# Optimization experiments

Measured on AMD Instinct MI355X. Metric: run time of the kernel, lower is better.

The kernel has to match this reference:

```python
import jax, jax.numpy as jnp
import numpy as np

B, S, D, H = 2, 2048, 1024, 16
DK = D // H

def setup_inputs() -> dict:
    key = jax.random.key(0)
    ks = jax.random.split(key, 12)
    s = 1.0 / np.sqrt(D)
    return {
        "q": jax.random.normal(ks[0], (B, S, D), jnp.float32),
        "k": jax.random.normal(ks[1], (B, S, D), jnp.float32),
        "v": jax.random.normal(ks[2], (B, S, D), jnp.float32),
        "mask": jnp.ones((1, 1, S, S), jnp.int32),
        "Wq": jax.random.normal(ks[3], (D, D), jnp.float32) * s,
        "bq": jnp.zeros((D,), jnp.float32),
        "Wk": jax.random.normal(ks[4], (D, D), jnp.float32) * s,
        "bk": jnp.zeros((D,), jnp.float32),
        "Wv": jax.random.normal(ks[5], (D, D), jnp.float32) * s,
        "bv": jnp.zeros((D,), jnp.float32),
        "Wo": jax.random.normal(ks[6], (D, D), jnp.float32) * s,
        "bo": jnp.zeros((D,), jnp.float32),
    }

def reference(q, k, v, mask, Wq, bq, Wk, bk, Wv, bv, Wo, bo):
    # projections (torch Linear: x @ W^T + b)
    Q = q @ Wq.T + bq
    K = k @ Wk.T + bk
    V = v @ Wv.T + bv
    # split heads: [B,S,D] -> [B,H,S,DK]
    def split(x):
        return x.reshape(B, S, H, DK).transpose(0, 2, 1, 3)
    Qh, Kh, Vh = split(Q), split(K), split(V)
    scores = jnp.einsum('bhqd,bhkd->bhqk', Qh, Kh) / jnp.sqrt(jnp.float32(DK))
    scores = jnp.where(mask == 0, jnp.float32(-1e9), scores)
    attn = jax.nn.softmax(scores, axis=-1)  # dropout p=0.0 -> identity
    x = jnp.einsum('bhqk,bhkd->bhqd', attn, Vh)
    x = x.transpose(0, 2, 1, 3).reshape(B, S, D)
    return x @ Wo.T + bo
```

## Files before the change

### kernel.cpp

```cpp
#include <hip/hip_runtime.h>
#include <hip/hip_bf16.h>
#include <stdint.h>

#define B_    2
#define S_    2048
#define D_    1024
#define H_    16
#define NTOK  (B_ * S_)

typedef __attribute__((ext_vector_type(8))) short bf16x8;
typedef __attribute__((ext_vector_type(4))) float f32x4;
typedef __attribute__((ext_vector_type(2))) float float2v;
typedef __attribute__((ext_vector_type(2))) __bf16 bfv2;

static __device__ __forceinline__ unsigned short f2bf(float f) {
    unsigned int u = __float_as_uint(f);
    unsigned int r = (u + 0x7FFFu + ((u >> 16) & 1u)) >> 16;
    return (unsigned short)r;
}
static __device__ __forceinline__ unsigned int pkbf(float a, float b) {
    float2v fv = {a, b};
    bfv2 r = __builtin_convertvector(fv, bfv2);
    unsigned int u;
    __builtin_memcpy(&u, &r, 4);
    return u;
}

using g_cu32 = __attribute__((address_space(1))) const unsigned int;
using l_u32  = __attribute__((address_space(3))) unsigned int;
static __device__ __forceinline__ void gld16(const void* g, void* l) {
    __builtin_amdgcn_global_load_lds((g_cu32*)g, (l_u32*)l, 16, 0, 0);
}

#define QN ((size_t)NTOK * D_)
#define WN ((size_t)D_ * D_)

__global__ __launch_bounds__(256) void prep_kernel(
    const float* __restrict__ q, const float* __restrict__ k, const float* __restrict__ v,
    const float* __restrict__ Wq, const float* __restrict__ Wk,
    const float* __restrict__ Wv, const float* __restrict__ Wo,
    const int* __restrict__ mask,
    unsigned short* __restrict__ qb, unsigned short* __restrict__ kb,
    unsigned short* __restrict__ vb, unsigned short* __restrict__ wqb,
    unsigned short* __restrict__ wkb, unsigned short* __restrict__ wvb,
    unsigned short* __restrict__ wob, int* __restrict__ flags) {
    __shared__ int anyz;
    if (blockIdx.x < 8192) {
        size_t i = ((size_t)blockIdx.x * 256 + threadIdx.x) * 8;
        const float* s; unsigned short* d; size_t off;
        if (i < QN)          { s = q; d = qb; off = i; }
        else if (i < 2 * QN) { s = k; d = kb; off = i - QN; }
        else if (i < 3 * QN) { s = v; d = vb; off = i - 2 * QN; }
        else {
            size_t j = i - 3 * QN;
            int wi = (int)(j >> 20);
            s = (wi == 0) ? Wq : (wi == 1) ? Wk : (wi == 2) ? Wv : Wo;
            d = (wi == 0) ? wqb : (wi == 1) ? wkb : (wi == 2) ? wvb : wob;
            off = j & (WN - 1);
        }
        float4 a = *(const float4*)(s + off);
        float4 b = *(const float4*)(s + off + 4);
        uint4 pk;
        pk.x = pkbf(a.x, a.y); pk.y = pkbf(a.z, a.w);
        pk.z = pkbf(b.x, b.y); pk.w = pkbf(b.z, b.w);
        *(uint4*)(d + off) = pk;
    } else {
        if (threadIdx.x == 0) anyz = 0;
        __syncthreads();
        int bid2 = blockIdx.x - 8192;
        const int qt = bid2 >> 5, kt = bid2 & 31;
        int az = 0;
        for (int i = threadIdx.x; i < 64 * 64; i += 256) {
            int r = i >> 6, c = i & 63;
            az |= (mask[(size_t)(qt * 64 + r) * S_ + kt * 64 + c] == 0) ? 1 : 0;
        }
        if (az) atomicOr(&anyz, 1);
        __syncthreads();
        if (threadIdx.x == 0) flags[qt * 32 + kt] = anyz;
    }
}

struct GemmArgs {
    const unsigned short* A[3];
    const unsigned short* W[3];
    const float* bias[3];
    void* C[3];
    int mode[3];
    float scale[3];
};

template<int BMT>
__global__ __launch_bounds__(256, 3) void gemm_async(GemmArgs ga) {
    constexpr int AG = BMT / 16;
    constexpr int MI = BMT / 32;
    const int z = blockIdx.z;
    const unsigned short* __restrict__ A = ga.A[z];
    const unsigned short* __restrict__ W = ga.W[z];
    const float* __restrict__ bias = ga.bias[z];
    void* C = ga.C[z];
    const int mode = ga.mode[z];
    const float scl = ga.scale[z];

    __shared__ unsigned short As[AG * 512];
    __shared__ unsigned short Bs[8 * 512];

    const int t    = threadIdx.x;
    const int lane = t & 63;
    const int w    = t >> 6;
    const int fr   = lane & 15;
    const int kq   = lane >> 4;
    const int wrow = w >> 1, wcol = w & 1;
    const int m0 = blockIdx.x * BMT, n0 = blockIdx.y * 128;

    const int sc = lane >> 4;
    const int sr = lane & 15;

    const unsigned short* ga0;
    const unsigned short* ga1 = nullptr;
    unsigned short* la0;
    unsigned short* la1 = nullptr;
    if constexpr (BMT == 128) {
        ga0 = A + (size_t)(m0 + (2 * w) * 16 + sr) * D_ + sc * 8;
        ga1 = ga0 + 16 * D_;
        la0 = &As[(2 * w) * 512];
        la1 = &As[(2 * w + 1) * 512];
    } else {
        ga0 = A + (size_t)(m0 + w * 16 + sr) * D_ + sc * 8;
        la0 = &As[w * 512];
    }
    const unsigned short* gw0 = W + (size_t)(n0 + (2 * w) * 16 + sr) * D_ + sc * 8;
    const unsigned short* gw1 = gw0 + 16 * D_;
    unsigned short* lw0 = &Bs[(2 * w) * 512];
    unsigned short* lw1 = &Bs[(2 * w + 1) * 512];

    int aOff[MI], bOff[4];
#pragma unroll
    for (int mi = 0; mi < MI; ++mi) aOff[mi] = (wrow * MI + mi) * 512 + (kq * 16 + fr) * 8;
#pragma unroll
    for (int ni = 0; ni < 4; ++ni) bOff[ni] = (wcol * 4 + ni) * 512 + (kq * 16 + fr) * 8;

    f32x4 acc[MI][4];
#pragma unroll
    for (int i = 0; i < MI; ++i)
#pragma unroll
        for (int j = 0; j < 4; ++j) acc[i][j] = (f32x4)0.0f;

    for (int k0 = 0; k0 < D_ / 32; ++k0) {
        gld16(ga0, la0);
        if constexpr (BMT == 128) gld16(ga1, la1);
        gld16(gw0, lw0);
        gld16(gw1, lw1);
        ga0 += 32; gw0 += 32; gw1 += 32;
        if constexpr (BMT == 128) ga1 += 32;
        __syncthreads();

        bf16x8 af[MI], bfr[4];
#pragma unroll
        for (int mi = 0; mi < MI; ++mi) af[mi] = *(const bf16x8*)&As[aOff[mi]];
#pragma unroll
        for (int ni = 0; ni < 4; ++ni) bfr[ni] = *(const bf16x8*)&Bs[bOff[ni]];
#pragma unroll
        for (int mi = 0; mi < MI; ++mi)
#pragma unroll
            for (int ni = 0; ni < 4; ++ni)
                acc[mi][ni] = __builtin_amdgcn_mfma_f32_16x16x32_bf16(
                    af[mi], bfr[ni], acc[mi][ni], 0, 0, 0);
        __syncthreads();
    }

    if (mode == 0) {
        float* Co = (float*)C;
#pragma unroll
        for (int ni = 0; ni < 4; ++ni) {
            int col = n0 + wcol * 64 + ni * 16 + fr;
            float bv = bias[col];
#pragma unroll
            for (int mi = 0; mi < MI; ++mi)
#pragma unroll
                for (int r = 0; r < 4; ++r) {
                    int row = m0 + wrow * (BMT / 2) + mi * 16 + kq * 4 + r;
                    Co[(size_t)row * D_ + col] = (acc[mi][ni][r] + bv) * scl;
                }
        }
    } else if (mode == 1) {
        unsigned short* Co = (unsigned short*)C;
#pragma unroll
        for (int ni = 0; ni < 4; ++ni) {
            int col = n0 + wcol * 64 + ni * 16 + fr;
            float bv = bias[col];
#pragma unroll
            for (int mi = 0; mi < MI; ++mi)
#pragma unroll
                for (int r = 0; r < 4; ++r) {
                    int row = m0 + wrow * (BMT / 2) + mi * 16 + kq * 4 + r;
                    Co[(size_t)row * D_ + col] = f2bf((acc[mi][ni][r] + bv) * scl);
                }
        }
    } else {
        unsigned short* Co = (unsigned short*)C;
#pragma unroll
        for (int ni = 0; ni < 4; ++ni) {
            int col = n0 + wcol * 64 + ni * 16 + fr;
            float bv = bias[col];
            int hh = col >> 6, d = col & 63;
#pragma unroll
            for (int mi = 0; mi < MI; ++mi) {
                int tok = m0 + wrow * (BMT / 2) + mi * 16 + kq * 4;
                int bb = tok >> 11, sbase = tok & (S_ - 1);
                uint2 pk;
                pk.x = pkbf((acc[mi][ni][0] + bv) * scl, (acc[mi][ni][1] + bv) * scl);
                pk.y = pkbf((acc[mi][ni][2] + bv) * scl, (acc[mi][ni][3] + bv) * scl);
                *(uint2*)(Co + ((size_t)((bb * H_ + hh) * 64 + d)) * S_ + sbase) = pk;
            }
        }
    }
}

__global__ __launch_bounds__(256, 4) void flash4(
    const unsigned short* __restrict__ Qb, const unsigned short* __restrict__ Kb,
    const unsigned short* __restrict__ Vtg, const int* __restrict__ mask,
    const int* __restrict__ flags, unsigned short* __restrict__ Xb) {
    __shared__ unsigned short Ks[2][4096];
    __shared__ unsigned short Vs[2][4096];
    __shared__ unsigned short Ps[4096];

    const int t    = threadIdx.x;
    const int lane = t & 63;
    const int w    = t >> 6;
    const int fr   = lane & 15;
    const int kq   = lane >> 4;
    const int qt = blockIdx.x, hd = blockIdx.y, b = blockIdx.z;
    const int q0 = qt * 64;
    const int swz = fr & 7;

    const unsigned short* qrow_p = Qb + (size_t)(b * S_ + q0 + w * 16 + fr) * D_ + hd * 64;
    bf16x8 qf[2];
    qf[0] = *(const bf16x8*)(qrow_p + kq * 8);
    qf[1] = *(const bf16x8*)(qrow_p + 32 + kq * 8);

    int fl = (lane < 32) ? flags[qt * 32 + lane] : 0;
    unsigned int fmask = (unsigned int)__ballot(fl != 0);

    const unsigned short* kbase =
        Kb + (size_t)(b * S_ + w * 16 + fr) * D_ + hd * 64 + kq * 8;
    const unsigned short* vbase =
        Vtg + ((size_t)((b * H_ + hd) * 64 + w * 16 + fr)) * S_ + kq * 8;

#pragma unroll
    for (int j = 0; j < 2; ++j) {
        gld16(kbase + j * 32, (char*)&Ks[0][0] + w * 2048 + j * 1024);
        gld16(vbase + j * 32, (char*)&Vs[0][0] + w * 2048 + j * 1024);
    }

    f32x4 o[4];
#pragma unroll
    for (int i = 0; i < 4; ++i) o[i] = (f32x4)0.0f;
    float l_i = 0.0f;

    for (int kt = 0; kt < 32; ++kt) {
        const int cur = kt & 1;
        __syncthreads();
        if (kt < 31) {
#pragma unroll
            for (int j = 0; j < 2; ++j) {
                gld16(kbase + (size_t)(kt + 1) * 64 * D_ + j * 32,
                      (char*)&Ks[cur ^ 1][0] + w * 2048 + j * 1024);
                gld16(vbase + (size_t)(kt + 1) * 64 + j * 32,
                      (char*)&Vs[cur ^ 1][0] + w * 2048 + j * 1024);
            }
        }

        f32x4 st[4];
#pragma unroll
        for (int mi = 0; mi < 4; ++mi) st[mi] = (f32x4)0.0f;
#pragma unroll
        for (int kk = 0; kk < 2; ++kk)
#pragma unroll
            for (int mi = 0; mi < 4; ++mi) {
                bf16x8 a = *(const bf16x8*)&Ks[cur][mi * 1024 + ((kk * 4 + kq) * 16 + fr) * 8];
                st[mi] = __builtin_amdgcn_mfma_f32_16x16x32_bf16(a, qf[kk], st[mi], 0, 0, 0);
            }

        if ((fmask >> kt) & 1u) {
#pragma unroll
            for (int mi = 0; mi < 4; ++mi) {
                int4 mv = *(const int4*)&mask[(size_t)(q0 + w * 16 + fr) * S_ + kt * 64 + mi * 16 + kq * 4];
                if (mv.x == 0) st[mi][0] = -3e8f;
                if (mv.y == 0) st[mi][1] = -3e8f;
                if (mv.z == 0) st[mi][2] = -3e8f;
                if (mv.w == 0) st[mi][3] = -3e8f;
            }
        }

#pragma unroll
        for (int mi = 0; mi < 4; ++mi) {
            float e0 = exp2f(st[mi][0]), e1 = exp2f(st[mi][1]);
            float e2 = exp2f(st[mi][2]), e3 = exp2f(st[mi][3]);
            l_i += (e0 + e1) + (e2 + e3);
            uint2 pk;
            pk.x = pkbf(e0, e1);
            pk.y = pkbf(e2, e3);
            int chunk = mi * 2 + (kq >> 1);
            *(uint2*)&Ps[(w * 16 + fr) * 64 + ((chunk ^ swz) << 3) + ((kq & 1) << 2)] = pk;
        }

#pragma unroll
        for (int kk = 0; kk < 2; ++kk) {
            int c = kk * 4 + kq;
            bf16x8 pb = *(const bf16x8*)&Ps[(w * 16 + fr) * 64 + ((c ^ swz) << 3)];
#pragma unroll
            for (int mi = 0; mi < 4; ++mi) {
                bf16x8 a = *(const bf16x8*)&Vs[cur][mi * 1024 + ((kk * 4 + kq) * 16 + fr) * 8];
                o[mi] = __builtin_amdgcn_mfma_f32_16x16x32_bf16(a, pb, o[mi], 0, 0, 0);
            }
        }
    }

    l_i += __shfl_xor(l_i, 16, 64);
    l_i += __shfl_xor(l_i, 32, 64);
    float rl = 1.0f / l_i;

#pragma unroll
    for (int mi = 0; mi < 4; ++mi) {
        uint2 pk;
        pk.x = pkbf(o[mi][0] * rl, o[mi][1] * rl);
        pk.y = pkbf(o[mi][2] * rl, o[mi][3] * rl);
        *(uint2*)(Xb + (size_t)(b * S_ + q0 + w * 16 + fr) * D_ + hd * 64 + mi * 16 + kq * 4) = pk;
    }
}

extern "C" void kernel_launch(void* const* d_in, const int* in_sizes, int n_in,
                              void* d_out, int out_size, void* d_ws, size_t ws_size,
                              hipStream_t stream) {
    const float* q    = (const float*)d_in[0];
    const float* k    = (const float*)d_in[1];
    const float* v    = (const float*)d_in[2];
    const int*   mask = (const int*)d_in[3];
    const float* Wq   = (const float*)d_in[4];
    const float* bq   = (const float*)d_in[5];
    const float* Wk   = (const float*)d_in[6];
    const float* bk   = (const float*)d_in[7];
    const float* Wv   = (const float*)d_in[8];
    const float* bv   = (const float*)d_in[9];
    const float* Wo   = (const float*)d_in[10];
    const float* bo   = (const float*)d_in[11];
    float* out = (float*)d_out;

    unsigned short* qb  = (unsigned short*)d_ws;
    unsigned short* kb  = qb + QN;
    unsigned short* vb  = kb + QN;
    unsigned short* Qf  = vb + QN;
    unsigned short* Kf  = Qf + QN;
    unsigned short* Vt  = Kf + QN;
    unsigned short* wqb = Vt + QN;
    unsigned short* wkb = wqb + WN;
    unsigned short* wvb = wkb + WN;
    unsigned short* wob = wvb + WN;
    int* flags = (int*)(wob + WN);

    const float SC = 0.18033688011112042f;

    prep_kernel<<<9216, 256, 0, stream>>>(q, k, v, Wq, Wk, Wv, Wo, mask,
                                          qb, kb, vb, wqb, wkb, wvb, wob, flags);

    GemmArgs g1;
    g1.A[0] = qb;  g1.W[0] = wqb; g1.bias[0] = bq; g1.C[0] = Qf; g1.mode[0] = 1; g1.scale[0] = SC;
    g1.A[1] = kb;  g1.W[1] = wkb; g1.bias[1] = bk; g1.C[1] = Kf; g1.mode[1] = 1; g1.scale[1] = 1.0f;
    g1.A[2] = vb;  g1.W[2] = wvb; g1.bias[2] = bv; g1.C[2] = Vt; g1.mode[2] = 2; g1.scale[2] = 1.0f;
    gemm_async<128><<<dim3(NTOK / 128, D_ / 128, 3), 256, 0, stream>>>(g1);

    flash4<<<dim3(S_ / 64, H_, B_), 256, 0, stream>>>(Qf, Kf, Vt, mask, flags, Qf);

    GemmArgs g2;
    g2.A[0] = Qf; g2.W[0] = wob; g2.bias[0] = bo; g2.C[0] = out; g2.mode[0] = 0; g2.scale[0] = 1.0f;
    g2.A[1] = g2.A[2] = nullptr; g2.W[1] = g2.W[2] = nullptr;
    g2.bias[1] = g2.bias[2] = nullptr; g2.C[1] = g2.C[2] = nullptr;
    g2.mode[1] = g2.mode[2] = 0; g2.scale[1] = g2.scale[2] = 1.0f;
    gemm_async<64><<<dim3(NTOK / 64, D_ / 128, 1), 256, 0, stream>>>(g2);
}
```

Baseline: 276.2 us.

## Enlarge attention blocks to 128 queries, swap GEMM MFMA operands for vector stores

The flash kernel now runs 512 threads (8 waves) per block covering 128 queries, so each staged K/V tile serves twice as many queries. Each wave loads one 16-byte chunk per tile, and the block index is remapped with a swizzle. Smaller edits switch to the hardware exp2, precompute the LDS P addresses and split the row-sum into a two-lane accumulator. In the GEMM, swapping the MFMA operands for modes 0 and 1 lets each lane write contiguous float4 or packed bf16 outputs and load bias as float4. The trade-offs are higher LDS use per block and a possible loss of occupancy.

```diff
diff --git a/kernel.cpp b/kernel.cpp
--- a/kernel.cpp
+++ b/kernel.cpp
@@ -13,11 +13,6 @@
 typedef __attribute__((ext_vector_type(2))) float float2v;
 typedef __attribute__((ext_vector_type(2))) __bf16 bfv2;
 
-static __device__ __forceinline__ unsigned short f2bf(float f) {
-    unsigned int u = __float_as_uint(f);
-    unsigned int r = (u + 0x7FFFu + ((u >> 16) & 1u)) >> 16;
-    return (unsigned short)r;
-}
 static __device__ __forceinline__ unsigned int pkbf(float a, float b) {
     float2v fv = {a, b};
     bfv2 r = __builtin_convertvector(fv, bfv2);
@@ -34,6 +29,9 @@
 
 #define QN ((size_t)NTOK * D_)
 #define WN ((size_t)D_ * D_)
+
+struct SwapT { static constexpr bool value = true; };
+struct NoSwapT { static constexpr bool value = false; };
 
 __global__ __launch_bounds__(256) void prep_kernel(
     const float* __restrict__ q, const float* __restrict__ k, const float* __restrict__ v,
@@ -145,58 +143,39 @@
 #pragma unroll
         for (int j = 0; j < 4; ++j) acc[i][j] = (f32x4)0.0f;
 
-    for (int k0 = 0; k0 < D_ / 32; ++k0) {
-        gld16(ga0, la0);
-        if constexpr (BMT == 128) gld16(ga1, la1);
-        gld16(gw0, lw0);
-        gld16(gw1, lw1);
-        ga0 += 32; gw0 += 32; gw1 += 32;
-        if constexpr (BMT == 128) ga1 += 32;
-        __syncthreads();
-
-        bf16x8 af[MI], bfr[4];
-#pragma unroll
-        for (int mi = 0; mi < MI; ++mi) af[mi] = *(const bf16x8*)&As[aOff[mi]];
-#pragma unroll
-        for (int ni = 0; ni < 4; ++ni) bfr[ni] = *(const bf16x8*)&Bs[bOff[ni]];
-#pragma unroll
-        for (int mi = 0; mi < MI; ++mi)
-#pragma unroll
-            for (int ni = 0; ni < 4; ++ni)
-                acc[mi][ni] = __builtin_amdgcn_mfma_f32_16x16x32_bf16(
-                    af[mi], bfr[ni], acc[mi][ni], 0, 0, 0);
-        __syncthreads();
-    }
-
-    if (mode == 0) {
-        float* Co = (float*)C;
-#pragma unroll
-        for (int ni = 0; ni < 4; ++ni) {
-            int col = n0 + wcol * 64 + ni * 16 + fr;
-            float bv = bias[col];
+    auto kloop = [&](auto swc) {
+        constexpr bool SW = decltype(swc)::value;
+        for (int k0 = 0; k0 < D_ / 32; ++k0) {
+            gld16(ga0, la0);
+            if constexpr (BMT == 128) gld16(ga1, la1);
+            gld16(gw0, lw0);
+            gld16(gw1, lw1);
+            ga0 += 32; gw0 += 32; gw1 += 32;
+            if constexpr (BMT == 128) ga1 += 32;
+            __syncthreads();
+
+            bf16x8 af[MI], bfr[4];
+#pragma unroll
+            for (int mi = 0; mi < MI; ++mi) af[mi] = *(const bf16x8*)&As[aOff[mi]];
+#pragma unroll
+            for (int ni = 0; ni < 4; ++ni) bfr[ni] = *(const bf16x8*)&Bs[bOff[ni]];
 #pragma unroll
             for (int mi = 0; mi < MI; ++mi)
 #pragma unroll
-                for (int r = 0; r < 4; ++r) {
-                    int row = m0 + wrow * (BMT / 2) + mi * 16 + kq * 4 + r;
-                    Co[(size_t)row * D_ + col] = (acc[mi][ni][r] + bv) * scl;
+                for (int ni = 0; ni < 4; ++ni) {
+                    if constexpr (SW)
+                        acc[mi][ni] = __builtin_amdgcn_mfma_f32_16x16x32_bf16(
+                            bfr[ni], af[mi], acc[mi][ni], 0, 0, 0);
+                    else
+                        acc[mi][ni] = __builtin_amdgcn_mfma_f32_16x16x32_bf16(
+                            af[mi], bfr[ni], acc[mi][ni], 0, 0, 0);
                 }
-        }
-    } else if (mode == 1) {
-        unsigned short* Co = (unsigned short*)C;
-#pragma unroll
-        for (int ni = 0; ni < 4; ++ni) {
-            int col = n0 + wcol * 64 + ni * 16 + fr;
-            float bv = bias[col];
-#pragma unroll
-            for (int mi = 0; mi < MI; ++mi)
-#pragma unroll
-                for (int r = 0; r < 4; ++r) {
-                    int row = m0 + wrow * (BMT / 2) + mi * 16 + kq * 4 + r;
-                    Co[(size_t)row * D_ + col] = f2bf((acc[mi][ni][r] + bv) * scl);
-                }
-        }
-    } else {
+            __syncthreads();
+        }
+    };
+    if (mode == 2) kloop(NoSwapT{}); else kloop(SwapT{});
+
+    if (mode == 2) {
         unsigned short* Co = (unsigned short*)C;
 #pragma unroll
         for (int ni = 0; ni < 4; ++ni) {
@@ -213,24 +192,58 @@
                 *(uint2*)(Co + ((size_t)((bb * H_ + hh) * 64 + d)) * S_ + sbase) = pk;
             }
         }
-    }
-}
-
-__global__ __launch_bounds__(256, 4) void flash4(
+    } else if (mode == 0) {
+        float* Co = (float*)C;
+#pragma unroll
+        for (int ni = 0; ni < 4; ++ni) {
+            int nb = n0 + wcol * 64 + ni * 16 + kq * 4;
+            float4 b4 = *(const float4*)&bias[nb];
+#pragma unroll
+            for (int mi = 0; mi < MI; ++mi) {
+                int m = m0 + wrow * (BMT / 2) + mi * 16 + fr;
+                float4 o4;
+                o4.x = (acc[mi][ni][0] + b4.x) * scl;
+                o4.y = (acc[mi][ni][1] + b4.y) * scl;
+                o4.z = (acc[mi][ni][2] + b4.z) * scl;
+                o4.w = (acc[mi][ni][3] + b4.w) * scl;
+                *(float4*)(Co + (size_t)m * D_ + nb) = o4;
+            }
+        }
+    } else {
+        unsigned short* Co = (unsigned short*)C;
+#pragma unroll
+        for (int ni = 0; ni < 4; ++ni) {
+            int nb = n0 + wcol * 64 + ni * 16 + kq * 4;
+            float4 b4 = *(const float4*)&bias[nb];
+#pragma unroll
+            for (int mi = 0; mi < MI; ++mi) {
+                int m = m0 + wrow * (BMT / 2) + mi * 16 + fr;
+                uint2 pk;
+                pk.x = pkbf((acc[mi][ni][0] + b4.x) * scl, (acc[mi][ni][1] + b4.y) * scl);
+                pk.y = pkbf((acc[mi][ni][2] + b4.z) * scl, (acc[mi][ni][3] + b4.w) * scl);
+                *(uint2*)(Co + (size_t)m * D_ + nb) = pk;
+            }
+        }
+    }
+}
+
+__global__ __launch_bounds__(512, 4) void flash4(
     const unsigned short* __restrict__ Qb, const unsigned short* __restrict__ Kb,
     const unsigned short* __restrict__ Vtg, const int* __restrict__ mask,
     const int* __restrict__ flags, unsigned short* __restrict__ Xb) {
     __shared__ unsigned short Ks[2][4096];
     __shared__ unsigned short Vs[2][4096];
-    __shared__ unsigned short Ps[4096];
+    __shared__ unsigned short Ps[8192];
 
     const int t    = threadIdx.x;
     const int lane = t & 63;
     const int w    = t >> 6;
     const int fr   = lane & 15;
     const int kq   = lane >> 4;
-    const int qt = blockIdx.x, hd = blockIdx.y, b = blockIdx.z;
-    const int q0 = qt * 64;
+    const int bid = blockIdx.x;
+    const int swb = ((bid & 7) << 6) | (bid >> 3);
+    const int qt = swb & 15, hd = (swb >> 4) & 15, b = swb >> 8;
+    const int q0 = qt * 128;
     const int swz = fr & 7;
 
     const unsigned short* qrow_p = Qb + (size_t)(b * S_ + q0 + w * 16 + fr) * D_ + hd * 64;
@@ -238,48 +251,59 @@
     qf[0] = *(const bf16x8*)(qrow_p + kq * 8);
     qf[1] = *(const bf16x8*)(qrow_p + 32 + kq * 8);
 
-    int fl = (lane < 32) ? flags[qt * 32 + lane] : 0;
+    int fl = (lane < 32) ? flags[(qt * 2 + (w >> 2)) * 32 + lane] : 0;
     unsigned int fmask = (unsigned int)__ballot(fl != 0);
 
-    const unsigned short* kbase =
-        Kb + (size_t)(b * S_ + w * 16 + fr) * D_ + hd * 64 + kq * 8;
-    const unsigned short* vbase =
-        Vtg + ((size_t)((b * H_ + hd) * 64 + w * 16 + fr)) * S_ + kq * 8;
-
-#pragma unroll
-    for (int j = 0; j < 2; ++j) {
-        gld16(kbase + j * 32, (char*)&Ks[0][0] + w * 2048 + j * 1024);
-        gld16(vbase + j * 32, (char*)&Vs[0][0] + w * 2048 + j * 1024);
-    }
-
+    const unsigned short* kptr =
+        Kb + (size_t)(b * S_ + (w >> 1) * 16 + fr) * D_ + hd * 64 + (w & 1) * 32 + kq * 8;
+    const unsigned short* vptr =
+        Vtg + ((size_t)((b * H_ + hd) * 64 + (w >> 1) * 16 + fr)) * S_ + (w & 1) * 32 + kq * 8;
+
+    gld16(kptr, (char*)&Ks[0][0] + w * 1024);
+    gld16(vptr, (char*)&Vs[0][0] + w * 1024);
+    const unsigned short* kpf = kptr + (size_t)64 * D_;
+    const unsigned short* vpf = vptr + 64;
+
+    unsigned short* pswr[4];
+#pragma unroll
+    for (int mi = 0; mi < 4; ++mi) {
+        int chunk = mi * 2 + (kq >> 1);
+        pswr[mi] = &Ps[(w * 16 + fr) * 64 + ((chunk ^ swz) << 3) + ((kq & 1) << 2)];
+    }
+    const unsigned short* psrd[2];
+#pragma unroll
+    for (int kk = 0; kk < 2; ++kk) {
+        int c = kk * 4 + kq;
+        psrd[kk] = &Ps[(w * 16 + fr) * 64 + ((c ^ swz) << 3)];
+    }
+
+    const f32x4 zf = (f32x4)0.0f;
     f32x4 o[4];
 #pragma unroll
-    for (int i = 0; i < 4; ++i) o[i] = (f32x4)0.0f;
-    float l_i = 0.0f;
+    for (int i = 0; i < 4; ++i) o[i] = zf;
+    float2v l2 = {0.0f, 0.0f};
 
     for (int kt = 0; kt < 32; ++kt) {
         const int cur = kt & 1;
         __syncthreads();
         if (kt < 31) {
-#pragma unroll
-            for (int j = 0; j < 2; ++j) {
-                gld16(kbase + (size_t)(kt + 1) * 64 * D_ + j * 32,
-                      (char*)&Ks[cur ^ 1][0] + w * 2048 + j * 1024);
-                gld16(vbase + (size_t)(kt + 1) * 64 + j * 32,
-                      (char*)&Vs[cur ^ 1][0] + w * 2048 + j * 1024);
-            }
+            gld16(kpf, (char*)&Ks[cur ^ 1][0] + w * 1024);
+            gld16(vpf, (char*)&Vs[cur ^ 1][0] + w * 1024);
+            kpf += (size_t)64 * D_;
+            vpf += 64;
         }
 
         f32x4 st[4];
 #pragma unroll
-        for (int mi = 0; mi < 4; ++mi) st[mi] = (f32x4)0.0f;
-#pragma unroll
-        for (int kk = 0; kk < 2; ++kk)
-#pragma unroll
-            for (int mi = 0; mi < 4; ++mi) {
-                bf16x8 a = *(const bf16x8*)&Ks[cur][mi * 1024 + ((kk * 4 + kq) * 16 + fr) * 8];
-                st[mi] = __builtin_amdgcn_mfma_f32_16x16x32_bf16(a, qf[kk], st[mi], 0, 0, 0);
-            }
+        for (int mi = 0; mi < 4; ++mi) {
+            bf16x8 a = *(const bf16x8*)&Ks[cur][mi * 1024 + (kq * 16 + fr) * 8];
+            st[mi] = __builtin_amdgcn_mfma_f32_16x16x32_bf16(a, qf[0], zf, 0, 0, 0);
+        }
+#pragma unroll
+        for (int mi = 0; mi < 4; ++mi) {
+            bf16x8 a = *(const bf16x8*)&Ks[cur][mi * 1024 + ((4 + kq) * 16 + fr) * 8];
+            st[mi] = __builtin_amdgcn_mfma_f32_16x16x32_bf16(a, qf[1], st[mi], 0, 0, 0);
+        }
 
         if ((fmask >> kt) & 1u) {
 #pragma unroll
@@ -294,20 +318,20 @@
 
 #pragma unroll
         for (int mi = 0; mi < 4; ++mi) {
-            float e0 = exp2f(st[mi][0]), e1 = exp2f(st[mi][1]);
-            float e2 = exp2f(st[mi][2]), e3 = exp2f(st[mi][3]);
-            l_i += (e0 + e1) + (e2 + e3);
+            float e0 = __builtin_amdgcn_exp2f(st[mi][0]);
+            float e1 = __builtin_amdgcn_exp2f(st[mi][1]);
+            float e2 = __builtin_amdgcn_exp2f(st[mi][2]);
+            float e3 = __builtin_amdgcn_exp2f(st[mi][3]);
+            l2 += (float2v){e0, e1} + (float2v){e2, e3};
             uint2 pk;
             pk.x = pkbf(e0, e1);
             pk.y = pkbf(e2, e3);
-            int chunk = mi * 2 + (kq >> 1);
-            *(uint2*)&Ps[(w * 16 + fr) * 64 + ((chunk ^ swz) << 3) + ((kq & 1) << 2)] = pk;
+            *(uint2*)pswr[mi] = pk;
         }
 
 #pragma unroll
         for (int kk = 0; kk < 2; ++kk) {
-            int c = kk * 4 + kq;
-            bf16x8 pb = *(const bf16x8*)&Ps[(w * 16 + fr) * 64 + ((c ^ swz) << 3)];
+            bf16x8 pb = *(const bf16x8*)psrd[kk];
 #pragma unroll
             for (int mi = 0; mi < 4; ++mi) {
                 bf16x8 a = *(const bf16x8*)&Vs[cur][mi * 1024 + ((kk * 4 + kq) * 16 + fr) * 8];
@@ -316,6 +340,7 @@
         }
     }
 
+    float l_i = l2.x + l2.y;
     l_i += __shfl_xor(l_i, 16, 64);
     l_i += __shfl_xor(l_i, 32, 64);
     float rl = 1.0f / l_i;
@@ -369,7 +394,7 @@
     g1.A[2] = vb;  g1.W[2] = wvb; g1.bias[2] = bv; g1.C[2] = Vt; g1.mode[2] = 2; g1.scale[2] = 1.0f;
     gemm_async<128><<<dim3(NTOK / 128, D_ / 128, 3), 256, 0, stream>>>(g1);
 
-    flash4<<<dim3(S_ / 64, H_, B_), 256, 0, stream>>>(Qf, Kf, Vt, mask, flags, Qf);
+    flash4<<<dim3((S_ / 128) * H_ * B_, 1, 1), 512, 0, stream>>>(Qf, Kf, Vt, mask, flags, Qf);
 
     GemmArgs g2;
     g2.A[0] = Qf; g2.W[0] = wob; g2.bias[0] = bo; g2.C[0] = out; g2.mode[0] = 0; g2.scale[0] = 1.0f;
```

Result: faster. 261.2 us (-5.4%).
